# Kernel tuning notes

Hardware: AMD Instinct MI355X
Metric: run time of the kernel (lower is better)

The kernel has to match this reference:

```python
import jax, jax.numpy as jnp
import numpy as np

B, S, D = 2, 2048, 1024
H, G = 16, 4
HD = D // H
E, K = 8, 2
F = 4 * D
EPS = 1e-6


def _ln(x, scale, bias):
    mu = jnp.mean(x, -1, keepdims=True)
    var = jnp.mean((x - mu) ** 2, -1, keepdims=True)
    return (x - mu) * jax.lax.rsqrt(var + EPS) * scale + bias


def setup_inputs() -> dict:
    key = jax.random.key(0)
    ks = jax.random.split(key, 12)
    p = lambda k, shape: jax.random.normal(k, shape, jnp.float32) * 0.02
    return dict(
        x=jax.random.normal(ks[0], (B, S, D), jnp.float32),
        session_deltas=jax.random.uniform(ks[1], (B, S), jnp.float32, 0.0, 100.0),
        ln1_scale=jnp.ones((D,), jnp.float32), ln1_bias=jnp.zeros((D,), jnp.float32),
        wq=p(ks[2], (D, H, HD)), bq=jnp.zeros((H, HD), jnp.float32),
        wk=p(ks[3], (D, G, HD)), bk=jnp.zeros((G, HD), jnp.float32),
        wv=p(ks[4], (D, G, HD)), bv=jnp.zeros((G, HD), jnp.float32),
        wo=p(ks[5], (H, HD, D)), bo=jnp.zeros((D,), jnp.float32),
        time_decay=jnp.zeros((H,), jnp.float32),
        ln2_scale=jnp.ones((D,), jnp.float32), ln2_bias=jnp.zeros((D,), jnp.float32),
        router_w=p(ks[6], (D, E)), router_b=jnp.zeros((E,), jnp.float32),
        w1=p(ks[7], (E, D, F)), b1=jnp.zeros((E, F), jnp.float32),
        w2=p(ks[8], (E, F, D)), b2=jnp.zeros((E, D), jnp.float32),
    )


def reference(x, session_deltas, ln1_scale, ln1_bias, wq, bq, wk, bk, wv, bv, wo, bo,
              time_decay, ln2_scale, ln2_bias, router_w, router_b, w1, b1, w2, b2):
    # ---- pre-norm time-aware GQA ----
    xn = _ln(x, ln1_scale, ln1_bias)
    q = jnp.einsum('bsd,dhk->bshk', xn, wq) + bq            # [B,S,H,HD]
    k = jnp.einsum('bsd,dgk->bsgk', xn, wk) + bk            # [B,S,G,HD]
    v = jnp.einsum('bsd,dgk->bsgk', xn, wv) + bv
    rep = H // G
    k = jnp.repeat(k, rep, axis=2)                          # [B,S,H,HD]
    v = jnp.repeat(v, rep, axis=2)
    scores = jnp.einsum('bqhk,bshk->bhqs', q, k) / np.float32(np.sqrt(HD))
    # session-delta-modulated scores: learned per-head temporal decay
    dt = jnp.abs(session_deltas[:, :, None] - session_deltas[:, None, :])  # [B,S,S]
    scores = scores - jax.nn.softplus(time_decay)[None, :, None, None] * dt[:, None, :, :]
    attn = jax.nn.softmax(scores, axis=-1)
    o = jnp.einsum('bhqs,bshk->bqhk', attn, v)
    attn_out = jnp.einsum('bqhk,hkd->bqd', o, wo) + bo
    x = x + attn_out
    # ---- pre-norm sparse MoE FFN ----
    xn2 = _ln(x, ln2_scale, ln2_bias)
    t = xn2.reshape(B * S, D)
    logits = t @ router_w + router_b                         # [T,E]
    probs = jax.nn.softmax(logits, axis=-1)
    topv, topi = jax.lax.top_k(probs, K)
    topv = topv / jnp.sum(topv, axis=-1, keepdims=True)
    combine = jnp.sum(jax.nn.one_hot(topi, E, dtype=t.dtype) * topv[..., None], axis=1)  # [T,E]
    h = jax.nn.gelu(jnp.einsum('td,edf->tef', t, w1) + b1)   # [T,E,F]
    y = jnp.einsum('tef,efd->ted', h, w2) + b2               # [T,E,D]
    moe_out = jnp.einsum('ted,te->td', y, combine).reshape(B, S, D)
    return x + moe_out
```

## Files before the change

### kernel.cpp

```cpp
#include <hip/hip_runtime.h>
#include <cstdint>
#include <cstddef>

typedef unsigned short u16;
typedef __bf16 bf16x8 __attribute__((ext_vector_type(8)));
typedef float f32x4 __attribute__((ext_vector_type(4)));

#define B_ 2
#define S_ 2048
#define D_ 1024
#define H_ 16
#define G_ 4
#define HD_ 64
#define E_ 8
#define F_ 4096
#define T_ 4096

__device__ __forceinline__ u16 f2b(float f) {
  unsigned u = __float_as_uint(f);
  return (u16)((u + 0x7fffu + ((u >> 16) & 1u)) >> 16);
}
__device__ __forceinline__ float b2f(u16 h) {
  return __uint_as_float(((unsigned)h) << 16);
}

__device__ __forceinline__ float gelu_t(float x) {
  float u = 0.7978845608028654f * (x + 0.044715f * x * x * x);
  float t = 1.f - 2.f / (__expf(2.f * u) + 1.f);
  return 0.5f * x * (1.f + t);
}

__device__ __forceinline__ void gload16(const void* g, void* l) {
  __builtin_amdgcn_global_load_lds((__attribute__((address_space(1))) void*)g,
                                   (__attribute__((address_space(3))) void*)l, 16, 0, 0);
}


__global__ void k_zero(int* cnt) {
  if (threadIdx.x < E_) cnt[threadIdx.x] = 0;
}

__global__ __launch_bounds__(256) void k_transpose(const float* __restrict__ src,
                                                   u16* __restrict__ dst, int R, int C) {
  __shared__ u16 tile[32][33];
  int c0 = blockIdx.x * 32, r0 = blockIdx.y * 32;
  size_t zo = (size_t)blockIdx.z * (size_t)R * (size_t)C;
  int tx = threadIdx.x, ty = threadIdx.y;
  #pragma unroll
  for (int i = ty; i < 32; i += 8) {
    int r = r0 + i, cc = c0 + tx;
    float v = (r < R && cc < C) ? src[zo + (size_t)r * C + cc] : 0.f;
    tile[i][tx] = f2b(v);
  }
  __syncthreads();
  #pragma unroll
  for (int i = ty; i < 32; i += 8) {
    int cc = c0 + i, r = r0 + tx;
    if (cc < C && r < R) dst[zo + (size_t)cc * R + r] = tile[tx][i];
  }
}

__global__ __launch_bounds__(256) void k_split_transpose(const float* __restrict__ src,
                                                         u16* __restrict__ dsth,
                                                         u16* __restrict__ dstl,
                                                         int R, int C) {
  __shared__ float tile[32][33];
  int c0 = blockIdx.x * 32, r0 = blockIdx.y * 32;
  int tx = threadIdx.x, ty = threadIdx.y;
  #pragma unroll
  for (int i = ty; i < 32; i += 8) {
    int r = r0 + i, cc = c0 + tx;
    tile[i][tx] = (r < R && cc < C) ? src[(size_t)r * C + cc] : 0.f;
  }
  __syncthreads();
  #pragma unroll
  for (int i = ty; i < 32; i += 8) {
    int cc = c0 + i, r = r0 + tx;
    if (cc < C && r < R) {
      float v = tile[tx][i];
      u16 h = f2b(v);
      dsth[(size_t)cc * R + r] = h;
      dstl[(size_t)cc * R + r] = f2b(v - b2f(h));
    }
  }
}

__global__ void k_prep_bias(const float* bq, const float* bk, const float* bv, float* bqkv) {
  int i = blockIdx.x * 256 + threadIdx.x;
  if (i < 1024) bqkv[i] = bq[i];
  else if (i < 1280) bqkv[i] = bk[i - 1024];
  else if (i < 1536) bqkv[i] = bv[i - 1280];
}

__global__ __launch_bounds__(256) void k_ln(const float* __restrict__ x,
                                            const float* __restrict__ sc,
                                            const float* __restrict__ bi,
                                            float* __restrict__ of,
                                            u16* __restrict__ ob,
                                            u16* __restrict__ oh,
                                            u16* __restrict__ ol) {
  int t = blockIdx.x, tid = threadIdx.x;
  const float* row = x + (size_t)t * D_;
  float4 v = *(const float4*)&row[tid * 4];
  float s = v.x + v.y + v.z + v.w;
  float ss = v.x * v.x + v.y * v.y + v.z * v.z + v.w * v.w;
  #pragma unroll
  for (int off = 32; off > 0; off >>= 1) {
    s += __shfl_xor(s, off);
    ss += __shfl_xor(ss, off);
  }
  __shared__ float red[8];
  if ((tid & 63) == 0) { red[(tid >> 6) * 2] = s; red[(tid >> 6) * 2 + 1] = ss; }
  __syncthreads();
  float S = red[0] + red[2] + red[4] + red[6];
  float SS = red[1] + red[3] + red[5] + red[7];
  float mu = S * (1.f / D_);
  float var = SS * (1.f / D_) - mu * mu;
  float rs = rsqrtf(var + 1e-6f);
  float4 scv = *(const float4*)&sc[tid * 4];
  float4 biv = *(const float4*)&bi[tid * 4];
  float o[4];
  o[0] = (v.x - mu) * rs * scv.x + biv.x;
  o[1] = (v.y - mu) * rs * scv.y + biv.y;
  o[2] = (v.z - mu) * rs * scv.z + biv.z;
  o[3] = (v.w - mu) * rs * scv.w + biv.w;
  size_t base = (size_t)t * D_ + tid * 4;
  if (of) *(float4*)&of[base] = make_float4(o[0], o[1], o[2], o[3]);
  if (ob) {
    ushort4 u;
    u.x = f2b(o[0]); u.y = f2b(o[1]); u.z = f2b(o[2]); u.w = f2b(o[3]);
    *(ushort4*)&ob[base] = u;
  }
  if (oh) {
    ushort4 uh, ulv;
    #pragma unroll
    for (int i = 0; i < 4; ++i) {
      u16 h = f2b(o[i]);
      u16 lo = f2b(o[i] - b2f(h));
      ((u16*)&uh)[i] = h;
      ((u16*)&ulv)[i] = lo;
    }
    *(ushort4*)&oh[base] = uh;
    *(ushort4*)&ol[base] = ulv;
  }
}

template <int OUTMODE>
__global__ __launch_bounds__(256) void k_gemm_split(const u16* __restrict__ Ah,
                                                    const u16* __restrict__ Al,
                                                    const u16* __restrict__ Bh,
                                                    const u16* __restrict__ Bl,
                                                    const float* __restrict__ bias,
                                                    const float* __restrict__ res,
                                                    u16* __restrict__ Ch,
                                                    u16* __restrict__ Cl,
                                                    float* __restrict__ Cf,
                                                    int M, int N, int K) {
  __shared__ __align__(16) u16 Ash[128 * 32], Asl[128 * 32];
  __shared__ __align__(16) u16 Bsh[128 * 32], Bsl[128 * 32];
  int tid = threadIdx.x, w = tid >> 6, l = tid & 63;
  int quad = l >> 4, l15 = l & 15;
  int m0 = blockIdx.x * 128, n0 = blockIdx.y * 128;
  int koff = (l & 3) * 8;
  const u16 *aph[2], *apl[2], *bph[2], *bpl[2];
  #pragma unroll
  for (int c = 0; c < 2; ++c) {
    int chunk = c * 4 + w;
    int row = m0 + chunk * 16 + (l >> 2);
    aph[c] = Ah + (size_t)row * K + koff;
    apl[c] = Al + (size_t)row * K + koff;
    int nrow = n0 + chunk * 16 + (l >> 2);
    bph[c] = Bh + (size_t)nrow * K + koff;
    bpl[c] = Bl + (size_t)nrow * K + koff;
  }
  f32x4 acc[4][4] = {};
  int wm = (w & 1) * 64, wn = (w >> 1) * 64;
  for (int k0 = 0; k0 < K; k0 += 32) {
    __syncthreads();
    #pragma unroll
    for (int c = 0; c < 2; ++c) {
      gload16(aph[c] + k0, &Ash[(c * 4 + w) * 512]);
      gload16(apl[c] + k0, &Asl[(c * 4 + w) * 512]);
      gload16(bph[c] + k0, &Bsh[(c * 4 + w) * 512]);
      gload16(bpl[c] + k0, &Bsl[(c * 4 + w) * 512]);
    }
    __syncthreads();
    bf16x8 ah[4], al_[4], bh[4], bl_[4];
    #pragma unroll
    for (int i = 0; i < 4; ++i) {
      ah[i] = *(const bf16x8*)&Ash[(wm + i * 16 + l15) * 32 + quad * 8];
      al_[i] = *(const bf16x8*)&Asl[(wm + i * 16 + l15) * 32 + quad * 8];
    }
    #pragma unroll
    for (int j = 0; j < 4; ++j) {
      bh[j] = *(const bf16x8*)&Bsh[(wn + j * 16 + l15) * 32 + quad * 8];
      bl_[j] = *(const bf16x8*)&Bsl[(wn + j * 16 + l15) * 32 + quad * 8];
    }
    #pragma unroll
    for (int i = 0; i < 4; ++i)
      #pragma unroll
      for (int j = 0; j < 4; ++j) {
        acc[i][j] = __builtin_amdgcn_mfma_f32_16x16x32_bf16(ah[i], bh[j], acc[i][j], 0, 0, 0);
        acc[i][j] = __builtin_amdgcn_mfma_f32_16x16x32_bf16(ah[i], bl_[j], acc[i][j], 0, 0, 0);
        acc[i][j] = __builtin_amdgcn_mfma_f32_16x16x32_bf16(al_[i], bh[j], acc[i][j], 0, 0, 0);
      }
  }
  #pragma unroll
  for (int i = 0; i < 4; ++i) {
    #pragma unroll
    for (int j = 0; j < 4; ++j) {
      int gn = n0 + wn + j * 16 + l15;
      float bv = bias[gn];
      #pragma unroll
      for (int r = 0; r < 4; ++r) {
        int gm = m0 + wm + i * 16 + quad * 4 + r;
        size_t idx = (size_t)gm * N + gn;
        float v = acc[i][j][r] + bv;
        if (OUTMODE == 0) {
          u16 h = f2b(v);
          Ch[idx] = h;
          Cl[idx] = f2b(v - b2f(h));
        } else {
          Cf[idx] = v + res[idx];
        }
      }
    }
  }
}

#define AP 72
__global__ __launch_bounds__(256) void k_attn_mfma(const u16* __restrict__ qkv_h,
                                                   const u16* __restrict__ qkv_l,
                                                   const float* __restrict__ sd,
                                                   const float* __restrict__ td,
                                                   u16* __restrict__ o_h,
                                                   u16* __restrict__ o_l) {
  __shared__ __align__(16) u16 Qh[64 * AP], Ql[64 * AP];
  __shared__ __align__(16) u16 Kh[64 * AP], Kl[64 * AP];
  __shared__ __align__(16) u16 Vth[64 * AP], Vtl[64 * AP];
  __shared__ __align__(16) u16 Ph[4][16 * AP], Pl[4][16 * AP];
  __shared__ float sds[64];
  int tid = threadIdx.x, w = tid >> 6, l = tid & 63;
  int quad = l >> 4, l15 = l & 15;
  int q0 = blockIdx.x * 64, h = blockIdx.y, b = blockIdx.z;
  int g = h >> 2;
  int r = tid >> 2, cb = (tid & 3) * 16;

  {
    const u16* gq_h = qkv_h + (size_t)(b * S_ + q0 + r) * 1536 + h * HD_ + cb;
    const u16* gq_l = qkv_l + (size_t)(b * S_ + q0 + r) * 1536 + h * HD_ + cb;
    #pragma unroll
    for (int c = 0; c < 4; ++c) {
      *(ushort4*)&Qh[r * AP + cb + c * 4] = *(const ushort4*)&gq_h[c * 4];
      *(ushort4*)&Ql[r * AP + cb + c * 4] = *(const ushort4*)&gq_l[c * 4];
    }
  }
  __syncthreads();
  bf16x8 aqh[2], aql[2];
  #pragma unroll
  for (int kk = 0; kk < 2; ++kk) {
    aqh[kk] = *(const bf16x8*)&Qh[(w * 16 + l15) * AP + kk * 32 + quad * 8];
    aql[kk] = *(const bf16x8*)&Ql[(w * 16 + l15) * AP + kk * 32 + quad * 8];
  }
  float sp = log1pf(__expf(td[h]));
  float dq[4];
  #pragma unroll
  for (int i = 0; i < 4; ++i) dq[i] = sd[b * S_ + q0 + w * 16 + quad * 4 + i];

  float mr[4], lr[4];
  f32x4 oa[4] = {};
  #pragma unroll
  for (int i = 0; i < 4; ++i) { mr[i] = -3.0e38f; lr[i] = 0.f; }

  for (int s0 = 0; s0 < S_; s0 += 64) {
    const u16* gk_h = qkv_h + (size_t)(b * S_ + s0 + r) * 1536 + 1024 + g * HD_ + cb;
    const u16* gk_l = qkv_l + (size_t)(b * S_ + s0 + r) * 1536 + 1024 + g * HD_ + cb;
    const u16* gv_h = qkv_h + (size_t)(b * S_ + s0 + r) * 1536 + 1280 + g * HD_ + cb;
    const u16* gv_l = qkv_l + (size_t)(b * S_ + s0 + r) * 1536 + 1280 + g * HD_ + cb;
    ushort4 kh4[4], kl4[4];
    u16 vh[16], vl[16];
    #pragma unroll
    for (int c = 0; c < 4; ++c) {
      kh4[c] = *(const ushort4*)&gk_h[c * 4];
      kl4[c] = *(const ushort4*)&gk_l[c * 4];
      *(ushort4*)&vh[c * 4] = *(const ushort4*)&gv_h[c * 4];
      *(ushort4*)&vl[c * 4] = *(const ushort4*)&gv_l[c * 4];
    }
    __syncthreads();
    #pragma unroll
    for (int c = 0; c < 4; ++c) {
      *(ushort4*)&Kh[r * AP + cb + c * 4] = kh4[c];
      *(ushort4*)&Kl[r * AP + cb + c * 4] = kl4[c];
    }
    #pragma unroll
    for (int i = 0; i < 16; ++i) {
      Vth[(cb + i) * AP + r] = vh[i];
      Vtl[(cb + i) * AP + r] = vl[i];
    }
    if (tid < 64) sds[tid] = sd[b * S_ + s0 + tid];
    __syncthreads();

    f32x4 sc[4] = {};
    #pragma unroll
    for (int j = 0; j < 4; ++j) {
      #pragma unroll
      for (int kk = 0; kk < 2; ++kk) {
        bf16x8 bkh = *(const bf16x8*)&Kh[(j * 16 + l15) * AP + kk * 32 + quad * 8];
        bf16x8 bkl = *(const bf16x8*)&Kl[(j * 16 + l15) * AP + kk * 32 + quad * 8];
        sc[j] = __builtin_amdgcn_mfma_f32_16x16x32_bf16(aqh[kk], bkh, sc[j], 0, 0, 0);
        sc[j] = __builtin_amdgcn_mfma_f32_16x16x32_bf16(aqh[kk], bkl, sc[j], 0, 0, 0);
        sc[j] = __builtin_amdgcn_mfma_f32_16x16x32_bf16(aql[kk], bkh, sc[j], 0, 0, 0);
      }
    }
    float ds_[4];
    #pragma unroll
    for (int j = 0; j < 4; ++j) ds_[j] = sds[j * 16 + l15];
    float s_[4][4];
    #pragma unroll
    for (int j = 0; j < 4; ++j)
      #pragma unroll
      for (int i = 0; i < 4; ++i)
        s_[j][i] = sc[j][i] * 0.125f - sp * fabsf(dq[i] - ds_[j]);
    float mx[4];
    #pragma unroll
    for (int i = 0; i < 4; ++i)
      mx[i] = fmaxf(fmaxf(s_[0][i], s_[1][i]), fmaxf(s_[2][i], s_[3][i]));
    #pragma unroll
    for (int d = 1; d < 16; d <<= 1)
      #pragma unroll
      for (int i = 0; i < 4; ++i) mx[i] = fmaxf(mx[i], __shfl_xor(mx[i], d));
    float al[4], rsum[4], p[4][4];
    #pragma unroll
    for (int i = 0; i < 4; ++i) {
      float mn = fmaxf(mr[i], mx[i]);
      al[i] = __expf(mr[i] - mn);
      mr[i] = mn;
      rsum[i] = 0.f;
      #pragma unroll
      for (int j = 0; j < 4; ++j) { p[j][i] = __expf(s_[j][i] - mn); rsum[i] += p[j][i]; }
    }
    #pragma unroll
    for (int d = 1; d < 16; d <<= 1)
      #pragma unroll
      for (int i = 0; i < 4; ++i) rsum[i] += __shfl_xor(rsum[i], d);
    #pragma unroll
    for (int i = 0; i < 4; ++i) {
      lr[i] = lr[i] * al[i] + rsum[i];
      #pragma unroll
      for (int j = 0; j < 4; ++j) oa[j][i] *= al[i];
    }
    #pragma unroll
    for (int j = 0; j < 4; ++j)
      #pragma unroll
      for (int i = 0; i < 4; ++i) {
        float pv = p[j][i];
        u16 hv = f2b(pv);
        Ph[w][(quad * 4 + i) * AP + j * 16 + l15] = hv;
        Pl[w][(quad * 4 + i) * AP + j * 16 + l15] = f2b(pv - b2f(hv));
      }
    bf16x8 aph[2], apl[2];
    #pragma unroll
    for (int kk = 0; kk < 2; ++kk) {
      aph[kk] = *(const bf16x8*)&Ph[w][l15 * AP + kk * 32 + quad * 8];
      apl[kk] = *(const bf16x8*)&Pl[w][l15 * AP + kk * 32 + quad * 8];
    }
    #pragma unroll
    for (int j = 0; j < 4; ++j) {
      #pragma unroll
      for (int kk = 0; kk < 2; ++kk) {
        bf16x8 bvh = *(const bf16x8*)&Vth[(j * 16 + l15) * AP + kk * 32 + quad * 8];
        bf16x8 bvl = *(const bf16x8*)&Vtl[(j * 16 + l15) * AP + kk * 32 + quad * 8];
        oa[j] = __builtin_amdgcn_mfma_f32_16x16x32_bf16(aph[kk], bvh, oa[j], 0, 0, 0);
        oa[j] = __builtin_amdgcn_mfma_f32_16x16x32_bf16(aph[kk], bvl, oa[j], 0, 0, 0);
        oa[j] = __builtin_amdgcn_mfma_f32_16x16x32_bf16(apl[kk], bvh, oa[j], 0, 0, 0);
      }
    }
  }
  #pragma unroll
  for (int i = 0; i < 4; ++i) {
    float inv = 1.f / lr[i];
    int q = b * S_ + q0 + w * 16 + quad * 4 + i;
    #pragma unroll
    for (int j = 0; j < 4; ++j) {
      float ov = oa[j][i] * inv;
      size_t idx = (size_t)q * (H_ * HD_) + h * HD_ + j * 16 + l15;
      u16 hv = f2b(ov);
      o_h[idx] = hv;
      o_l[idx] = f2b(ov - b2f(hv));
    }
  }
}

__global__ __launch_bounds__(256) void k_router(const float* __restrict__ xn2,
                                                const float* __restrict__ rw,
                                                const float* __restrict__ rb,
                                                int* __restrict__ eidx, int* __restrict__ epos,
                                                float* __restrict__ ew, int* __restrict__ cnt,
                                                int* __restrict__ list) {
  int t = blockIdx.x * 4 + (threadIdx.x >> 6);
  int l = threadIdx.x & 63;
  const float* row = xn2 + (size_t)t * D_;
  float acc[8];
  #pragma unroll
  for (int e = 0; e < 8; ++e) acc[e] = 0.f;
  for (int i = 0; i < 16; ++i) {
    int d = l + i * 64;
    float xv = row[d];
    float4 w0 = *(const float4*)&rw[d * 8 + 0];
    float4 w1 = *(const float4*)&rw[d * 8 + 4];
    acc[0] = fmaf(xv, w0.x, acc[0]); acc[1] = fmaf(xv, w0.y, acc[1]);
    acc[2] = fmaf(xv, w0.z, acc[2]); acc[3] = fmaf(xv, w0.w, acc[3]);
    acc[4] = fmaf(xv, w1.x, acc[4]); acc[5] = fmaf(xv, w1.y, acc[5]);
    acc[6] = fmaf(xv, w1.z, acc[6]); acc[7] = fmaf(xv, w1.w, acc[7]);
  }
  #pragma unroll
  for (int off = 32; off > 0; off >>= 1)
    #pragma unroll
    for (int e = 0; e < 8; ++e) acc[e] += __shfl_xor(acc[e], off);
  if (l == 0) {
    float lg[8];
    #pragma unroll
    for (int e = 0; e < 8; ++e) lg[e] = acc[e] + rb[e];
    int i1 = 0;
    #pragma unroll
    for (int e = 1; e < 8; ++e) if (lg[e] > lg[i1]) i1 = e;
    int i2 = (i1 == 0) ? 1 : 0;
    #pragma unroll
    for (int e = 0; e < 8; ++e) if (e != i1 && lg[e] > lg[i2]) i2 = e;
    float wa = 1.f / (1.f + __expf(lg[i2] - lg[i1]));
    float wb = 1.f - wa;
    int pa = atomicAdd(&cnt[i1], 1);
    int pb = atomicAdd(&cnt[i2], 1);
    list[i1 * T_ + pa] = t;
    list[i2 * T_ + pb] = t;
    eidx[2 * t] = i1; eidx[2 * t + 1] = i2;
    epos[2 * t] = pa; epos[2 * t + 1] = pb;
    ew[2 * t] = wa; ew[2 * t + 1] = wb;
  }
}

__global__ void k_offsets(const int* __restrict__ cnt, int* __restrict__ offs) {
  if (threadIdx.x == 0 && blockIdx.x == 0) {
    int tot = 0, ttot = 0;
    for (int e = 0; e < E_; ++e) {
      offs[e] = tot; tot += cnt[e];
      offs[8 + e] = ttot; ttot += (cnt[e] + 127) >> 7;
    }
    offs[16] = ttot;
  }
}

__global__ __launch_bounds__(128) void k_gather(const u16* __restrict__ src,
                                                const int* __restrict__ offs,
                                                const int* __restrict__ list,
                                                u16* __restrict__ dst) {
  int s = blockIdx.x;
  int e = 0;
  #pragma unroll
  for (int i = 1; i < E_; ++i) e = (s >= offs[i]) ? i : e;
  int tok = list[e * T_ + (s - offs[e])];
  int l = threadIdx.x;
  ushort4 a = *(const ushort4*)&src[(size_t)tok * D_ + l * 8];
  ushort4 b = *(const ushort4*)&src[(size_t)tok * D_ + l * 8 + 4];
  *(ushort4*)&dst[(size_t)s * D_ + l * 8] = a;
  *(ushort4*)&dst[(size_t)s * D_ + l * 8 + 4] = b;
}

template <int MODE, int LOGNY>
__global__ __launch_bounds__(256) void k_moe_gemm(const u16* __restrict__ Ab,
                                                  const u16* __restrict__ Wt,
                                                  const float* __restrict__ bias,
                                                  u16* __restrict__ outU,
                                                  const int* __restrict__ cnt,
                                                  const int* __restrict__ meta,
                                                  int N, int K) {
  int q = gridDim.x >> 3;
  int wid = (blockIdx.x & 7) * q + (blockIdx.x >> 3);
  int tx = wid >> LOGNY;
  int ny = wid & ((1 << LOGNY) - 1);
  if (tx >= meta[16]) return;
  int e = 0;
  #pragma unroll
  for (int i = 1; i < E_; ++i) e = (tx >= meta[8 + i]) ? i : e;
  int myM = cnt[e];
  int m0 = (tx - meta[8 + e]) * 128;
  int n0 = ny * 128;
  __shared__ __align__(16) u16 As[3][128 * 32];
  __shared__ __align__(16) u16 Bs[3][128 * 32];
  int tid = threadIdx.x, w = tid >> 6, l = tid & 63;
  int quad = l >> 4, l15 = l & 15;
  int koff = (l & 3) * 8;
  const u16* ap[2];
  const u16* bp[2];
  #pragma unroll
  for (int c = 0; c < 2; ++c) {
    int chunk = c * 4 + w;
    int r = m0 + chunk * 16 + (l >> 2);
    int rr = (r < myM) ? r : (myM - 1);
    ap[c] = Ab + (size_t)(meta[e] + rr) * K + koff;
    int nrow = n0 + chunk * 16 + (l >> 2);
    bp[c] = Wt + (size_t)e * N * K + (size_t)nrow * K + koff;
  }
  f32x4 acc[4][4] = {};
  int wm = (w & 1) * 64, wn = (w >> 1) * 64;
  int nsteps = K >> 5;
  #pragma unroll
  for (int c = 0; c < 2; ++c) {
    gload16(ap[c], &As[0][(c * 4 + w) * 512]);
    gload16(bp[c], &Bs[0][(c * 4 + w) * 512]);
  }
  #pragma unroll
  for (int c = 0; c < 2; ++c) {
    gload16(ap[c] + 32, &As[1][(c * 4 + w) * 512]);
    gload16(bp[c] + 32, &Bs[1][(c * 4 + w) * 512]);
  }
  int cur = 0, stg = 2;
  for (int it = 0; it < nsteps - 1; ++it) {
    asm volatile("s_waitcnt vmcnt(4)" ::: "memory");
    asm volatile("s_barrier" ::: "memory");
    if (it < nsteps - 2) {
      int k0 = (it + 2) << 5;
      #pragma unroll
      for (int c = 0; c < 2; ++c) {
        gload16(ap[c] + k0, &As[stg][(c * 4 + w) * 512]);
        gload16(bp[c] + k0, &Bs[stg][(c * 4 + w) * 512]);
      }
    }
    bf16x8 af[4], bfv[4];
    #pragma unroll
    for (int i = 0; i < 4; ++i)
      af[i] = *(const bf16x8*)&As[cur][(wm + i * 16 + l15) * 32 + quad * 8];
    #pragma unroll
    for (int j = 0; j < 4; ++j)
      bfv[j] = *(const bf16x8*)&Bs[cur][(wn + j * 16 + l15) * 32 + quad * 8];
    __builtin_amdgcn_s_setprio(1);
    #pragma unroll
    for (int i = 0; i < 4; ++i)
      #pragma unroll
      for (int j = 0; j < 4; ++j)
        acc[i][j] = __builtin_amdgcn_mfma_f32_16x16x32_bf16(af[i], bfv[j], acc[i][j], 0, 0, 0);
    __builtin_amdgcn_s_setprio(0);
    cur = (cur == 2) ? 0 : cur + 1;
    stg = (stg == 2) ? 0 : stg + 1;
  }
  asm volatile("s_waitcnt vmcnt(0)" ::: "memory");
  asm volatile("s_barrier" ::: "memory");
  {
    bf16x8 af[4], bfv[4];
    #pragma unroll
    for (int i = 0; i < 4; ++i)
      af[i] = *(const bf16x8*)&As[cur][(wm + i * 16 + l15) * 32 + quad * 8];
    #pragma unroll
    for (int j = 0; j < 4; ++j)
      bfv[j] = *(const bf16x8*)&Bs[cur][(wn + j * 16 + l15) * 32 + quad * 8];
    __builtin_amdgcn_s_setprio(1);
    #pragma unroll
    for (int i = 0; i < 4; ++i)
      #pragma unroll
      for (int j = 0; j < 4; ++j)
        acc[i][j] = __builtin_amdgcn_mfma_f32_16x16x32_bf16(af[i], bfv[j], acc[i][j], 0, 0, 0);
    __builtin_amdgcn_s_setprio(0);
  }
  const float* bptr = bias + (size_t)e * N;
  #pragma unroll
  for (int i = 0; i < 4; ++i) {
    #pragma unroll
    for (int j = 0; j < 4; ++j) {
      int gn = n0 + wn + j * 16 + l15;
      float bv = bptr[gn];
      #pragma unroll
      for (int r = 0; r < 4; ++r) {
        int gm = m0 + wm + i * 16 + quad * 4 + r;
        if (gm < myM) {
          float vv = acc[i][j][r] + bv;
          if (MODE == 0) vv = gelu_t(vv);
          outU[(size_t)(meta[e] + gm) * N + gn] = f2b(vv);
        }
      }
    }
  }
}

__global__ __launch_bounds__(256) void k_combine(const float* __restrict__ x1,
                                                 const u16* __restrict__ y,
                                                 const int* __restrict__ eidx,
                                                 const int* __restrict__ epos,
                                                 const float* __restrict__ ew,
                                                 const int* __restrict__ offs,
                                                 float* __restrict__ out) {
  int t = blockIdx.x, tid = threadIdx.x;
  int e0 = eidx[2 * t], e1 = eidx[2 * t + 1];
  int s0 = offs[e0] + epos[2 * t];
  int s1 = offs[e1] + epos[2 * t + 1];
  float w0 = ew[2 * t], w1 = ew[2 * t + 1];
  int d = tid * 4;
  float4 a = *(const float4*)&x1[(size_t)t * D_ + d];
  ushort4 y0 = *(const ushort4*)&y[(size_t)s0 * D_ + d];
  ushort4 y1 = *(const ushort4*)&y[(size_t)s1 * D_ + d];
  float4 r;
  r.x = a.x + w0 * b2f(y0.x) + w1 * b2f(y1.x);
  r.y = a.y + w0 * b2f(y0.y) + w1 * b2f(y1.y);
  r.z = a.z + w0 * b2f(y0.z) + w1 * b2f(y1.z);
  r.w = a.w + w0 * b2f(y0.w) + w1 * b2f(y1.w);
  *(float4*)&out[(size_t)t * D_ + d] = r;
}

extern "C" void kernel_launch(void* const* d_in, const int* in_sizes, int n_in,
                              void* d_out, int out_size, void* d_ws, size_t ws_size,
                              hipStream_t stream) {
  (void)in_sizes; (void)n_in; (void)out_size; (void)ws_size;
  const float* x    = (const float*)d_in[0];
  const float* sd   = (const float*)d_in[1];
  const float* ln1s = (const float*)d_in[2];
  const float* ln1b = (const float*)d_in[3];
  const float* wq   = (const float*)d_in[4];
  const float* bq   = (const float*)d_in[5];
  const float* wk   = (const float*)d_in[6];
  const float* bk   = (const float*)d_in[7];
  const float* wv   = (const float*)d_in[8];
  const float* bv   = (const float*)d_in[9];
  const float* wo   = (const float*)d_in[10];
  const float* bo   = (const float*)d_in[11];
  const float* td   = (const float*)d_in[12];
  const float* ln2s = (const float*)d_in[13];
  const float* ln2b = (const float*)d_in[14];
  const float* rw   = (const float*)d_in[15];
  const float* rb   = (const float*)d_in[16];
  const float* w1   = (const float*)d_in[17];
  const float* b1   = (const float*)d_in[18];
  const float* w2   = (const float*)d_in[19];
  const float* b2   = (const float*)d_in[20];
  float* out = (float*)d_out;

  const size_t MBy = 1024ull * 1024ull;
  char* ws = (char*)d_ws;
  u16*   w1t   = (u16*)(ws + 0);
  u16*   w2t   = (u16*)(ws + 64 * MBy);
  u16*   hb    = (u16*)(ws + 128 * MBy);
  float* xn2   = (float*)(ws + 128 * MBy);
  u16*   wqkvTh= (u16*)(ws + 192 * MBy);
  u16*   wqkvTl= (u16*)(ws + 195 * MBy);
  u16*   woTh  = (u16*)(ws + 198 * MBy);
  u16*   woTl  = (u16*)(ws + 200 * MBy);
  float* bqkv  = (float*)(ws + 202 * MBy);
  int*   eidx  = (int*)(ws + 202 * MBy + 65536);
  int*   epos  = eidx + 2 * T_;
  float* ew    = (float*)(epos + 2 * T_);
  int*   list  = (int*)(ew + 2 * T_);
  int*   cnt   = list + E_ * T_;
  int*   offs  = cnt + E_;
  u16*   xn_h  = (u16*)(ws + 203 * MBy);
  u16*   xn_l  = (u16*)(ws + 211 * MBy);
  u16*   xn2b  = (u16*)(ws + 203 * MBy);
  u16*   qkv_h = (u16*)(ws + 219 * MBy);
  u16*   qkv_l = (u16*)(ws + 232 * MBy);
  u16*   yb    = (u16*)(ws + 219 * MBy);
  u16*   o_h   = (u16*)(ws + 245 * MBy);
  u16*   o_l   = (u16*)(ws + 253 * MBy);
  u16*   aprime= (u16*)(ws + 245 * MBy);
  float* x1    = (float*)(ws + 261 * MBy);

  k_zero<<<1, 64, 0, stream>>>(cnt);
  k_transpose<<<dim3(F_ / 32, D_ / 32, E_), dim3(32, 8), 0, stream>>>(w1, w1t, D_, F_);
  k_transpose<<<dim3(D_ / 32, F_ / 32, E_), dim3(32, 8), 0, stream>>>(w2, w2t, F_, D_);
  k_split_transpose<<<dim3(1024 / 32, 1024 / 32), dim3(32, 8), 0, stream>>>(wq, wqkvTh, wqkvTl, 1024, 1024);
  k_split_transpose<<<dim3(256 / 32, 1024 / 32), dim3(32, 8), 0, stream>>>(wk, wqkvTh + 1024 * 1024, wqkvTl + 1024 * 1024, 1024, 256);
  k_split_transpose<<<dim3(256 / 32, 1024 / 32), dim3(32, 8), 0, stream>>>(wv, wqkvTh + 1280 * 1024, wqkvTl + 1280 * 1024, 1024, 256);
  k_split_transpose<<<dim3(1024 / 32, 1024 / 32), dim3(32, 8), 0, stream>>>(wo, woTh, woTl, 1024, 1024);
  k_prep_bias<<<6, 256, 0, stream>>>(bq, bk, bv, bqkv);

  k_ln<<<T_, 256, 0, stream>>>(x, ln1s, ln1b, nullptr, nullptr, xn_h, xn_l);

  k_gemm_split<0><<<dim3(T_ / 128, 1536 / 128), 256, 0, stream>>>(
      xn_h, xn_l, wqkvTh, wqkvTl, bqkv, nullptr, qkv_h, qkv_l, nullptr, T_, 1536, 1024);

  k_attn_mfma<<<dim3(S_ / 64, H_, B_), 256, 0, stream>>>(qkv_h, qkv_l, sd, td, o_h, o_l);

  k_gemm_split<1><<<dim3(T_ / 128, 1024 / 128), 256, 0, stream>>>(
      o_h, o_l, woTh, woTl, bo, x, nullptr, nullptr, x1, T_, 1024, 1024);

  k_ln<<<T_, 256, 0, stream>>>(x1, ln2s, ln2b, xn2, xn2b, nullptr, nullptr);

  k_router<<<T_ / 4, 256, 0, stream>>>(xn2, rw, rb, eidx, epos, ew, cnt, list);
  k_offsets<<<1, 64, 0, stream>>>(cnt, offs);
  k_gather<<<2 * T_, 128, 0, stream>>>(xn2b, offs, list, aprime);

  k_moe_gemm<0, 5><<<dim3(72 * 32), 256, 0, stream>>>(aprime, w1t, b1, hb, cnt, offs, F_, D_);
  k_moe_gemm<1, 3><<<dim3(72 * 8), 256, 0, stream>>>(hb, w2t, b2, yb, cnt, offs, D_, F_);

  k_combine<<<T_, 256, 0, stream>>>(x1, yb, eidx, epos, ew, offs, out);
}
```

Before: 1.101 ms.

## Pre-transpose V in a separate kernel and vectorize attention LDS writes

A new k_vt kernel transposes V once per (batch, KV group) into a [D, S] layout, with key positions permuted. The attention inner loop can then fill its V tile with vector LDS stores instead of 32 scalar transposed stores per thread per iteration. The P tile is written in the same permuted key order using packed uint2 stores, so the P·V product stays consistent. Session deltas are read straight into registers instead of going through shared memory, and s_setprio wraps the MFMA sections. The cost is two extra small kernel launches and extra workspace traffic for the transposed V.

```diff
diff --git a/kernel.cpp b/kernel.cpp
--- a/kernel.cpp
+++ b/kernel.cpp
@@ -228,9 +228,37 @@
   }
 }
 
+__global__ __launch_bounds__(256) void k_vt(const u16* __restrict__ qkv,
+                                            u16* __restrict__ vt) {
+  __shared__ u16 tile[64][72];
+  int bg = blockIdx.y;
+  int b = bg >> 2, g = bg & 3;
+  int s0 = blockIdx.x * 64;
+  int tid = threadIdx.x;
+  int r = tid >> 2, cb = (tid & 3) * 16;
+  const u16* src = qkv + (size_t)(b * S_ + s0 + r) * 1536 + 1280 + g * HD_ + cb;
+  int pr = ((r & 15) * 4) | (r >> 4);
+  #pragma unroll
+  for (int c = 0; c < 4; ++c) {
+    ushort4 v = *(const ushort4*)&src[c * 4];
+    tile[cb + c * 4 + 0][pr] = v.x;
+    tile[cb + c * 4 + 1][pr] = v.y;
+    tile[cb + c * 4 + 2][pr] = v.z;
+    tile[cb + c * 4 + 3][pr] = v.w;
+  }
+  __syncthreads();
+  int d = tid >> 2, scol = (tid & 3) * 16;
+  u16* dst = vt + ((size_t)bg * HD_ + d) * S_ + s0 + scol;
+  #pragma unroll
+  for (int c = 0; c < 4; ++c)
+    *(ushort4*)&dst[c * 4] = *(const ushort4*)&tile[d][scol + c * 4];
+}
+
 #define AP 72
 __global__ __launch_bounds__(256) void k_attn_mfma(const u16* __restrict__ qkv_h,
                                                    const u16* __restrict__ qkv_l,
+                                                   const u16* __restrict__ vth_g,
+                                                   const u16* __restrict__ vtl_g,
                                                    const float* __restrict__ sd,
                                                    const float* __restrict__ td,
                                                    u16* __restrict__ o_h,
@@ -239,11 +267,11 @@
   __shared__ __align__(16) u16 Kh[64 * AP], Kl[64 * AP];
   __shared__ __align__(16) u16 Vth[64 * AP], Vtl[64 * AP];
   __shared__ __align__(16) u16 Ph[4][16 * AP], Pl[4][16 * AP];
-  __shared__ float sds[64];
   int tid = threadIdx.x, w = tid >> 6, l = tid & 63;
   int quad = l >> 4, l15 = l & 15;
   int q0 = blockIdx.x * 64, h = blockIdx.y, b = blockIdx.z;
   int g = h >> 2;
+  int bg = b * G_ + g;
   int r = tid >> 2, cb = (tid & 3) * 16;
 
   {
@@ -275,32 +303,31 @@
   for (int s0 = 0; s0 < S_; s0 += 64) {
     const u16* gk_h = qkv_h + (size_t)(b * S_ + s0 + r) * 1536 + 1024 + g * HD_ + cb;
     const u16* gk_l = qkv_l + (size_t)(b * S_ + s0 + r) * 1536 + 1024 + g * HD_ + cb;
-    const u16* gv_h = qkv_h + (size_t)(b * S_ + s0 + r) * 1536 + 1280 + g * HD_ + cb;
-    const u16* gv_l = qkv_l + (size_t)(b * S_ + s0 + r) * 1536 + 1280 + g * HD_ + cb;
-    ushort4 kh4[4], kl4[4];
-    u16 vh[16], vl[16];
+    const u16* gvt_h = vth_g + ((size_t)bg * HD_ + r) * S_ + s0 + cb;
+    const u16* gvt_l = vtl_g + ((size_t)bg * HD_ + r) * S_ + s0 + cb;
+    ushort4 kh4[4], kl4[4], vth4[4], vtl4[4];
     #pragma unroll
     for (int c = 0; c < 4; ++c) {
       kh4[c] = *(const ushort4*)&gk_h[c * 4];
       kl4[c] = *(const ushort4*)&gk_l[c * 4];
-      *(ushort4*)&vh[c * 4] = *(const ushort4*)&gv_h[c * 4];
-      *(ushort4*)&vl[c * 4] = *(const ushort4*)&gv_l[c * 4];
-    }
+      vth4[c] = *(const ushort4*)&gvt_h[c * 4];
+      vtl4[c] = *(const ushort4*)&gvt_l[c * 4];
+    }
+    float dsv[4];
+    #pragma unroll
+    for (int j = 0; j < 4; ++j) dsv[j] = sd[b * S_ + s0 + j * 16 + l15];
     __syncthreads();
     #pragma unroll
     for (int c = 0; c < 4; ++c) {
       *(ushort4*)&Kh[r * AP + cb + c * 4] = kh4[c];
       *(ushort4*)&Kl[r * AP + cb + c * 4] = kl4[c];
-    }
-    #pragma unroll
-    for (int i = 0; i < 16; ++i) {
-      Vth[(cb + i) * AP + r] = vh[i];
-      Vtl[(cb + i) * AP + r] = vl[i];
-    }
-    if (tid < 64) sds[tid] = sd[b * S_ + s0 + tid];
+      *(ushort4*)&Vth[r * AP + cb + c * 4] = vth4[c];
+      *(ushort4*)&Vtl[r * AP + cb + c * 4] = vtl4[c];
+    }
     __syncthreads();
 
     f32x4 sc[4] = {};
+    __builtin_amdgcn_s_setprio(1);
     #pragma unroll
     for (int j = 0; j < 4; ++j) {
       #pragma unroll
@@ -312,15 +339,13 @@
         sc[j] = __builtin_amdgcn_mfma_f32_16x16x32_bf16(aql[kk], bkh, sc[j], 0, 0, 0);
       }
     }
-    float ds_[4];
-    #pragma unroll
-    for (int j = 0; j < 4; ++j) ds_[j] = sds[j * 16 + l15];
+    __builtin_amdgcn_s_setprio(0);
     float s_[4][4];
     #pragma unroll
     for (int j = 0; j < 4; ++j)
       #pragma unroll
       for (int i = 0; i < 4; ++i)
-        s_[j][i] = sc[j][i] * 0.125f - sp * fabsf(dq[i] - ds_[j]);
+        s_[j][i] = sc[j][i] * 0.125f - sp * fabsf(dq[i] - dsv[j]);
     float mx[4];
     #pragma unroll
     for (int i = 0; i < 4; ++i)
@@ -350,20 +375,26 @@
       for (int j = 0; j < 4; ++j) oa[j][i] *= al[i];
     }
     #pragma unroll
-    for (int j = 0; j < 4; ++j)
-      #pragma unroll
-      for (int i = 0; i < 4; ++i) {
-        float pv = p[j][i];
-        u16 hv = f2b(pv);
-        Ph[w][(quad * 4 + i) * AP + j * 16 + l15] = hv;
-        Pl[w][(quad * 4 + i) * AP + j * 16 + l15] = f2b(pv - b2f(hv));
-      }
+    for (int i = 0; i < 4; ++i) {
+      u16 h0 = f2b(p[0][i]), h1 = f2b(p[1][i]), h2 = f2b(p[2][i]), h3 = f2b(p[3][i]);
+      uint2 ph2;
+      ph2.x = (unsigned)h0 | ((unsigned)h1 << 16);
+      ph2.y = (unsigned)h2 | ((unsigned)h3 << 16);
+      *(uint2*)&Ph[w][(quad * 4 + i) * AP + l15 * 4] = ph2;
+      u16 e0 = f2b(p[0][i] - b2f(h0)), e1 = f2b(p[1][i] - b2f(h1));
+      u16 e2 = f2b(p[2][i] - b2f(h2)), e3 = f2b(p[3][i] - b2f(h3));
+      uint2 pl2;
+      pl2.x = (unsigned)e0 | ((unsigned)e1 << 16);
+      pl2.y = (unsigned)e2 | ((unsigned)e3 << 16);
+      *(uint2*)&Pl[w][(quad * 4 + i) * AP + l15 * 4] = pl2;
+    }
     bf16x8 aph[2], apl[2];
     #pragma unroll
     for (int kk = 0; kk < 2; ++kk) {
       aph[kk] = *(const bf16x8*)&Ph[w][l15 * AP + kk * 32 + quad * 8];
       apl[kk] = *(const bf16x8*)&Pl[w][l15 * AP + kk * 32 + quad * 8];
     }
+    __builtin_amdgcn_s_setprio(1);
     #pragma unroll
     for (int j = 0; j < 4; ++j) {
       #pragma unroll
@@ -375,6 +406,7 @@
         oa[j] = __builtin_amdgcn_mfma_f32_16x16x32_bf16(apl[kk], bvh, oa[j], 0, 0, 0);
       }
     }
+    __builtin_amdgcn_s_setprio(0);
   }
   #pragma unroll
   for (int i = 0; i < 4; ++i) {
@@ -638,6 +670,8 @@
   u16*   w2t   = (u16*)(ws + 64 * MBy);
   u16*   hb    = (u16*)(ws + 128 * MBy);
   float* xn2   = (float*)(ws + 128 * MBy);
+  u16*   vth   = (u16*)(ws + 128 * MBy);
+  u16*   vtl   = (u16*)(ws + 131 * MBy);
   u16*   wqkvTh= (u16*)(ws + 192 * MBy);
   u16*   wqkvTl= (u16*)(ws + 195 * MBy);
   u16*   woTh  = (u16*)(ws + 198 * MBy);
@@ -674,7 +708,10 @@
   k_gemm_split<0><<<dim3(T_ / 128, 1536 / 128), 256, 0, stream>>>(
       xn_h, xn_l, wqkvTh, wqkvTl, bqkv, nullptr, qkv_h, qkv_l, nullptr, T_, 1536, 1024);
 
-  k_attn_mfma<<<dim3(S_ / 64, H_, B_), 256, 0, stream>>>(qkv_h, qkv_l, sd, td, o_h, o_l);
+  k_vt<<<dim3(S_ / 64, B_ * G_), 256, 0, stream>>>(qkv_h, vth);
+  k_vt<<<dim3(S_ / 64, B_ * G_), 256, 0, stream>>>(qkv_l, vtl);
+
+  k_attn_mfma<<<dim3(S_ / 64, H_, B_), 256, 0, stream>>>(qkv_h, qkv_l, vth, vtl, sd, td, o_h, o_l);
 
   k_gemm_split<1><<<dim3(T_ / 128, 1024 / 128), 256, 0, stream>>>(
       o_h, o_l, woTh, woTl, bo, x, nullptr, nullptr, x1, T_, 1024, 1024);
```

Result: faster. 1.064 ms (-3.3%).
